# Kernel optimization log

Hardware: AMD Instinct MI355X
Metric: run time of the kernel (lower is better)

## Reference

```python
import jax, jax.numpy as jnp
import numpy as np


def _gtconv(A, w):
    # A: [E,N,N], w: [C,E,1,1]; torch: sum(A * softmax(w, dim=1), dim=1) -> [C,N,N]
    s = jax.nn.softmax(w[:, :, 0, 0], axis=1)  # [C,E]
    return jnp.einsum('enm,ce->cnm', A, s)


def _norm_row(H):
    # row-normalize (H + I): D^-1 (H + I)
    n = H.shape[0]
    H = H + jnp.eye(n, dtype=H.dtype)
    deg = jnp.sum(H, axis=1)
    deg = jnp.where(deg <= 1e-10, 1.0, deg)
    return H / deg[:, None]


def _sgc(feature, adj):
    # D^-1/2 (adj + 2I) D^-1/2 @ feature  (diag scaling, same math as torch's dense mm with diag)
    n = adj.shape[0]
    adj = adj + 2.0 * jnp.eye(n, dtype=adj.dtype)
    deg = jnp.sum(adj, axis=1)
    deg = jnp.where(deg <= 1e-10, 1.0, deg)
    dinv = deg ** -0.5
    adj = adj * dinv[:, None] * dinv[None, :]
    return adj @ feature


def setup_inputs() -> dict:
    key = jax.random.key(0)
    ks = jax.random.split(key, 20)
    E, C, N, D, P, F = 5, 2, 3000, 1000, 2000, 128
    inp = {
        'A': jax.random.uniform(ks[0], (E, N, N), dtype=jnp.float32),
        'DTI': jax.random.uniform(ks[1], (N, N), dtype=jnp.float32),
        'drug_structure': jax.random.normal(ks[2], (D, F), dtype=jnp.float32),
        'protein_structure': jax.random.normal(ks[3], (P, F), dtype=jnp.float32),
        'gt_w0a': jax.random.normal(ks[4], (C, E, 1, 1), dtype=jnp.float32),
        'gt_w0b': jax.random.normal(ks[5], (C, E, 1, 1), dtype=jnp.float32),
        'gt_w1': jax.random.normal(ks[6], (C, E, 1, 1), dtype=jnp.float32),
        'a_param': jnp.ones((C + 1, 1, 1), dtype=jnp.float32),
        'drug_num': D,
        'protein_num': P,
    }
    lin_keys = jax.random.split(ks[7], 12)
    names = ['wd1', 'bd1', 'wd2', 'bd2', 'wd3', 'bd3', 'wp1', 'bp1', 'wp2', 'bp2', 'wp3', 'bp3']
    for i, nm in enumerate(names):
        shp = (F, F) if nm.startswith('w') else (F,)
        inp[nm] = jax.random.normal(lin_keys[i], shp, dtype=jnp.float32) * 0.05
    return inp


def reference(A, DTI, drug_structure, protein_structure, gt_w0a, gt_w0b, gt_w1,
              wd1, bd1, wd2, bd2, wd3, bd3, wp1, bp1, wp2, bp2, wp3, bp3,
              a_param, drug_num, protein_num):
    relu = jax.nn.relu
    drug = relu(drug_structure @ wd1.T + bd1)
    drug = relu(drug @ wd2.T + bd2)
    drug = relu(drug @ wd3.T + bd3)
    prot = relu(protein_structure @ wp1.T + bp1)
    prot = relu(prot @ wp2.T + bp2)
    prot = relu(prot @ wp3.T + bp3)
    feature = jnp.concatenate([drug, prot], axis=0)  # [N,128]

    # GT layers: layer 0 (first=True), layer 1 (first=False)
    a0 = _gtconv(A, gt_w0a)  # [C,N,N]
    b0 = _gtconv(A, gt_w0b)
    H = jnp.matmul(a0, b0)  # bmm
    H = jax.vmap(_norm_row)(H)
    H = jnp.matmul(H, _gtconv(A, gt_w1))

    adj = H  # H[:, :N, :N] is a no-op here
    X_conv1 = _sgc(_sgc(feature, DTI), DTI)
    chs = jax.vmap(lambda a_: _sgc(_sgc(feature, a_), a_))(adj)  # [C,N,128]

    C = adj.shape[0]
    if C == 1:
        X_conv3 = chs
    else:
        order = [0, 1]
        for i in range(2, C):
            order = [i] + order  # torch prepends X_tem for i>=2
        X_conv3 = chs[jnp.array(order)]

    X_conv = jnp.concatenate([X_conv1[None], X_conv3], axis=0)  # [C+1,N,128]
    att = jax.nn.softmax(a_param, axis=0)  # [C+1,1,1]
    conv_sum = jnp.sum(att * X_conv, axis=0)  # [N,128]

    drug_feature = conv_sum[:drug_num]
    protein_feature = conv_sum[drug_num:]
    y = jax.nn.sigmoid(drug_feature @ protein_feature.T)  # [D,P]
    return y
```

## Files before the change

### kernel.cpp

```cpp
#include <hip/hip_runtime.h>
#include <hip/hip_bf16.h>

typedef __attribute__((ext_vector_type(8))) __bf16 bf16x8;
typedef __attribute__((ext_vector_type(4))) float floatx4;

#define NVALID 3000
#define NPAD   3072
#define FEA    128
#define ZSPLIT 8
#define KCHUNK 384
#define PSTRIDE 393216
#define SLOT   ((size_t)ZSPLIT * PSTRIDE)

__device__ __forceinline__ void gload16(const void* g, void* l) {
    __builtin_amdgcn_global_load_lds(
        (const __attribute__((address_space(1))) void*)g,
        (__attribute__((address_space(3))) void*)l,
        16, 0, 0);
}

__device__ __forceinline__ float b2f(__hip_bfloat16 h) { return __bfloat162float(h); }

__global__ __launch_bounds__(256) void mlp_fused(
    const float* __restrict__ Xd, const float* __restrict__ Xp,
    const float* __restrict__ Wd1, const float* __restrict__ bd1,
    const float* __restrict__ Wd2, const float* __restrict__ bd2,
    const float* __restrict__ Wd3, const float* __restrict__ bd3,
    const float* __restrict__ Wp1, const float* __restrict__ bp1,
    const float* __restrict__ Wp2, const float* __restrict__ bp2,
    const float* __restrict__ Wp3, const float* __restrict__ bp3,
    float* __restrict__ Y)
{
    const bool isP = blockIdx.x >= 125;
    const float* X  = isP ? Xp : Xd;
    const float* W1 = isP ? Wp1 : Wd1; const float* b1 = isP ? bp1 : bd1;
    const float* W2 = isP ? Wp2 : Wd2; const float* b2 = isP ? bp2 : bd2;
    const float* W3 = isP ? Wp3 : Wd3; const float* b3 = isP ? bp3 : bd3;
    const int m0loc = (isP ? (blockIdx.x - 125) : blockIdx.x) * 8;
    const int m0out = blockIdx.x * 8;

    __shared__ float S0[8][128], S1[8][128];
    const int t = threadIdx.x;
    for (int s2 = t; s2 < 1024; s2 += 256) {
        int r = s2 >> 7, ii = s2 & 127;
        S0[r][ii] = X[(size_t)(m0loc + r) * 128 + ii];
    }
    __syncthreads();
    const int o = t & 127, rh = t >> 7;

    {
        float a0 = 0.f, a1 = 0.f, a2 = 0.f, a3 = 0.f;
        const float* wr = W1 + (size_t)o * 128;
        for (int i = 0; i < 128; ++i) {
            float w = wr[i];
            a0 += S0[rh + 0][i] * w; a1 += S0[rh + 2][i] * w;
            a2 += S0[rh + 4][i] * w; a3 += S0[rh + 6][i] * w;
        }
        float bo = b1[o];
        S1[rh + 0][o] = fmaxf(a0 + bo, 0.f);
        S1[rh + 2][o] = fmaxf(a1 + bo, 0.f);
        S1[rh + 4][o] = fmaxf(a2 + bo, 0.f);
        S1[rh + 6][o] = fmaxf(a3 + bo, 0.f);
    }
    __syncthreads();
    {
        float a0 = 0.f, a1 = 0.f, a2 = 0.f, a3 = 0.f;
        const float* wr = W2 + (size_t)o * 128;
        for (int i = 0; i < 128; ++i) {
            float w = wr[i];
            a0 += S1[rh + 0][i] * w; a1 += S1[rh + 2][i] * w;
            a2 += S1[rh + 4][i] * w; a3 += S1[rh + 6][i] * w;
        }
        float bo = b2[o];
        S0[rh + 0][o] = fmaxf(a0 + bo, 0.f);
        S0[rh + 2][o] = fmaxf(a1 + bo, 0.f);
        S0[rh + 4][o] = fmaxf(a2 + bo, 0.f);
        S0[rh + 6][o] = fmaxf(a3 + bo, 0.f);
    }
    __syncthreads();
    {
        float a0 = 0.f, a1 = 0.f, a2 = 0.f, a3 = 0.f;
        const float* wr = W3 + (size_t)o * 128;
        for (int i = 0; i < 128; ++i) {
            float w = wr[i];
            a0 += S0[rh + 0][i] * w; a1 += S0[rh + 2][i] * w;
            a2 += S0[rh + 4][i] * w; a3 += S0[rh + 6][i] * w;
        }
        float bo = b3[o];
        Y[(size_t)(m0out + rh + 0) * 128 + o] = fmaxf(a0 + bo, 0.f);
        Y[(size_t)(m0out + rh + 2) * 128 + o] = fmaxf(a1 + bo, 0.f);
        Y[(size_t)(m0out + rh + 4) * 128 + o] = fmaxf(a2 + bo, 0.f);
        Y[(size_t)(m0out + rh + 6) * 128 + o] = fmaxf(a3 + bo, 0.f);
    }
}

__device__ __forceinline__ void softmax5(const float* __restrict__ w, float* s)
{
    float m = w[0];
    #pragma unroll
    for (int e = 1; e < 5; ++e) m = fmaxf(m, w[e]);
    float sum = 0.f;
    #pragma unroll
    for (int e = 0; e < 5; ++e) { s[e] = __expf(w[e] - m); sum += s[e]; }
    float r = 1.f / sum;
    #pragma unroll
    for (int e = 0; e < 5; ++e) s[e] *= r;
}

__global__ __launch_bounds__(256) void gtconv_stream(
    const float* __restrict__ A, const float* __restrict__ w0a,
    const float* __restrict__ w0b, const float* __restrict__ w1,
    __hip_bfloat16* __restrict__ a00, __hip_bfloat16* __restrict__ b00,
    __hip_bfloat16* __restrict__ g10,
    __hip_bfloat16* __restrict__ a01, __hip_bfloat16* __restrict__ b01,
    __hip_bfloat16* __restrict__ g11)
{
    float sa0[5], sb0[5], sg0[5], sa1[5], sb1[5], sg1[5];
    softmax5(w0a + 0, sa0); softmax5(w0b + 0, sb0); softmax5(w1 + 0, sg0);
    softmax5(w0a + 5, sa1); softmax5(w0b + 5, sb1); softmax5(w1 + 5, sg1);

    const int i  = blockIdx.y;
    const int j0 = blockIdx.x * 1024 + threadIdx.x * 4;
    float acc[6][4] = {};
    if (i < NVALID && j0 < NVALID) {
        const bool fast = (j0 + 3) < NVALID;
        #pragma unroll
        for (int e = 0; e < 5; ++e) {
            const float* Ae = A + (size_t)e * 9000000 + (size_t)i * 3000;
            float x[4];
            if (fast) {
                float4 v = *reinterpret_cast<const float4*>(Ae + j0);
                x[0] = v.x; x[1] = v.y; x[2] = v.z; x[3] = v.w;
            } else {
                #pragma unroll
                for (int u = 0; u < 4; ++u)
                    x[u] = (j0 + u < NVALID) ? Ae[j0 + u] : 0.f;
            }
            #pragma unroll
            for (int u = 0; u < 4; ++u) {
                acc[0][u] += sa0[e] * x[u];
                acc[1][u] += sb0[e] * x[u];
                acc[2][u] += sg0[e] * x[u];
                acc[3][u] += sa1[e] * x[u];
                acc[4][u] += sb1[e] * x[u];
                acc[5][u] += sg1[e] * x[u];
            }
        }
    }
    __hip_bfloat16* dsts[6] = { a00, b00, g10, a01, b01, g11 };
    const size_t base = (size_t)i * NPAD + j0;
    #pragma unroll
    for (int m = 0; m < 6; ++m) {
        __align__(8) __hip_bfloat16 h[4];
        #pragma unroll
        for (int u = 0; u < 4; ++u) h[u] = __float2bfloat16(acc[m][u]);
        *reinterpret_cast<uint2*>(&dsts[m][base]) = *reinterpret_cast<const uint2*>(h);
    }
}

__global__ __launch_bounds__(256) void rowsum4(
    const __hip_bfloat16* __restrict__ M0, const __hip_bfloat16* __restrict__ M1,
    const __hip_bfloat16* __restrict__ M2, const __hip_bfloat16* __restrict__ M3,
    float* __restrict__ r1v)
{
    const __hip_bfloat16* M = (blockIdx.y == 0) ? M0 : (blockIdx.y == 1) ? M1
                            : (blockIdx.y == 2) ? M2 : M3;
    const size_t i = blockIdx.x;
    const int t = threadIdx.x;
    const __hip_bfloat16* row = M + i * NPAD;
    float s = 0.f;
    for (int k = t * 8; k < NPAD; k += 2048) {
        uint4 u = *reinterpret_cast<const uint4*>(&row[k]);
        const unsigned short* us = reinterpret_cast<const unsigned short*>(&u);
        #pragma unroll
        for (int e = 0; e < 8; ++e)
            s += __uint_as_float(((unsigned int)us[e]) << 16);
    }
    #pragma unroll
    for (int off = 32; off > 0; off >>= 1) s += __shfl_down(s, off);
    __shared__ float red[4];
    if ((t & 63) == 0) red[t >> 6] = s;
    __syncthreads();
    if (t == 0)
        r1v[(size_t)blockIdx.y * NPAD + i] = red[0] + red[1] + red[2] + red[3];
}

__global__ __launch_bounds__(256) void matvec_degA(
    const __hip_bfloat16* __restrict__ a0_0, const __hip_bfloat16* __restrict__ a0_1,
    const __hip_bfloat16* __restrict__ b0_0, const __hip_bfloat16* __restrict__ b0_1,
    const float* __restrict__ r1v,
    float* __restrict__ dinv2, float* __restrict__ mv12)
{
    const int y = blockIdx.y;
    const __hip_bfloat16* M = (y == 0) ? a0_0 : (y == 1) ? a0_1 : (y == 2) ? b0_0 : b0_1;
    const float* v = (y == 0) ? r1v : (y == 1) ? r1v + 2 * NPAD
                   : (y == 2) ? r1v + NPAD : r1v + 3 * NPAD;
    const size_t i = blockIdx.x;
    const int t = threadIdx.x;
    const __hip_bfloat16* row = M + i * NPAD;
    float s = 0.f;
    for (int k = t * 8; k < NPAD; k += 2048) {
        uint4 u = *reinterpret_cast<const uint4*>(&row[k]);
        const unsigned short* us = reinterpret_cast<const unsigned short*>(&u);
        #pragma unroll
        for (int e = 0; e < 8; ++e)
            s += __uint_as_float(((unsigned int)us[e]) << 16) * v[k + e];
    }
    #pragma unroll
    for (int off = 32; off > 0; off >>= 1) s += __shfl_down(s, off);
    __shared__ float red[4];
    if ((t & 63) == 0) red[t >> 6] = s;
    __syncthreads();
    if (t == 0) {
        float tot = red[0] + red[1] + red[2] + red[3];
        if (y < 2) dinv2[(size_t)y * NPAD + i] = 1.f / (tot + 1.f);
        else       mv12[(size_t)(y - 2) * NPAD + i] = tot;
    }
}

__global__ __launch_bounds__(256) void matvec_degB(
    const __hip_bfloat16* __restrict__ a0_0, const __hip_bfloat16* __restrict__ a0_1,
    const float* __restrict__ mv12, const float* __restrict__ dinv2,
    const float* __restrict__ r1v, float* __restrict__ rsv2)
{
    const int c = blockIdx.y;
    const __hip_bfloat16* M = c ? a0_1 : a0_0;
    const float* v = mv12 + (size_t)c * NPAD;
    const float* add = r1v + (size_t)(2 * c + 1) * NPAD;
    const size_t i = blockIdx.x;
    const int t = threadIdx.x;
    const __hip_bfloat16* row = M + i * NPAD;
    float s = 0.f;
    for (int k = t * 8; k < NPAD; k += 2048) {
        uint4 u = *reinterpret_cast<const uint4*>(&row[k]);
        const unsigned short* us = reinterpret_cast<const unsigned short*>(&u);
        #pragma unroll
        for (int e = 0; e < 8; ++e)
            s += __uint_as_float(((unsigned int)us[e]) << 16) * v[k + e];
    }
    #pragma unroll
    for (int off = 32; off > 0; off >>= 1) s += __shfl_down(s, off);
    __shared__ float red[4];
    if ((t & 63) == 0) red[t >> 6] = s;
    __syncthreads();
    if (t == 0) {
        float tot = red[0] + red[1] + red[2] + red[3];
        rsv2[(size_t)c * NPAD + i] =
            rsqrtf(dinv2[(size_t)c * NPAD + i] * (tot + add[i]) + 2.f);
    }
}

__global__ __launch_bounds__(256) void rowdeg_f32(
    const float* __restrict__ src, float* __restrict__ outv)
{
    const int i = blockIdx.x, t = threadIdx.x;
    float s = 0.f;
    if (i < NVALID) {
        const float* row = src + (size_t)i * 3000;
        for (int j4 = t; j4 < 750; j4 += 256) {
            float4 v = *reinterpret_cast<const float4*>(row + j4 * 4);
            s += v.x + v.y + v.z + v.w;
        }
    }
    #pragma unroll
    for (int off = 32; off > 0; off >>= 1) s += __shfl_down(s, off);
    __shared__ float red[4];
    if ((t & 63) == 0) red[t >> 6] = s;
    __syncthreads();
    if (t == 0) {
        float tot = red[0] + red[1] + red[2] + red[3];
        outv[i] = rsqrtf(tot + 2.f);
    }
}

__global__ __launch_bounds__(256) void scale_cast_f32(
    const float* __restrict__ src, int lds_, int nvalid,
    const float* __restrict__ vec, __hip_bfloat16* __restrict__ dst)
{
    const int i = blockIdx.y;
    const int j0 = (blockIdx.x * 256 + threadIdx.x) * 4;
    const float vi = vec[i];
    float v[4];
    if (i < nvalid && j0 + 3 < nvalid) {
        float4 f = *reinterpret_cast<const float4*>(src + (size_t)i * lds_ + j0);
        v[0] = f.x; v[1] = f.y; v[2] = f.z; v[3] = f.w;
    } else {
        #pragma unroll
        for (int u = 0; u < 4; ++u) {
            int j = j0 + u;
            v[u] = (i < nvalid && j < nvalid) ? src[(size_t)i * lds_ + j] : 0.f;
        }
    }
    #pragma unroll
    for (int u = 0; u < 4; ++u) {
        int j = j0 + u;
        if (j == i && i < nvalid) v[u] += 2.f;
        v[u] *= vi * vec[j];
    }
    __align__(8) __hip_bfloat16 h[4];
    #pragma unroll
    for (int u = 0; u < 4; ++u) h[u] = __float2bfloat16(v[u]);
    *reinterpret_cast<uint2*>(&dst[(size_t)i * NPAD + j0]) =
        *reinterpret_cast<const uint2*>(h);
}

__global__ __launch_bounds__(256) void transpose_feat(
    const float* __restrict__ X, int nvalid, __hip_bfloat16* __restrict__ XT)
{
    __shared__ float Ts[32][33];
    const int k0 = blockIdx.x * 32, n0 = blockIdx.y * 32;
    const int t = threadIdx.x, tr = t >> 5, tc = t & 31;
    #pragma unroll
    for (int p = 0; p < 4; ++p) {
        int k = k0 + tr + p * 8;
        Ts[tr + p * 8][tc] = (k < nvalid) ? X[(size_t)k * 128 + n0 + tc] : 0.f;
    }
    __syncthreads();
    #pragma unroll
    for (int p = 0; p < 4; ++p) {
        int n = tr + p * 8;
        XT[(size_t)(n0 + n) * NPAD + k0 + tc] = __float2bfloat16(Ts[tc][n]);
    }
}

__global__ __launch_bounds__(256) void scale_colsT2(
    const __hip_bfloat16* __restrict__ XT, const float* __restrict__ rsv2,
    __hip_bfloat16* __restrict__ W0T_0, __hip_bfloat16* __restrict__ W0T_1)
{
    const int c = blockIdx.z;
    const float* s = rsv2 + (size_t)c * NPAD;
    __hip_bfloat16* W0T = c ? W0T_1 : W0T_0;
    const int f = blockIdx.y;
    const int k0 = (blockIdx.x * 256 + threadIdx.x) * 8;
    if (k0 >= NPAD) return;
    uint4 u = *reinterpret_cast<const uint4*>(&XT[(size_t)f * NPAD + k0]);
    const unsigned short* us = reinterpret_cast<const unsigned short*>(&u);
    __align__(16) __hip_bfloat16 h[8];
    #pragma unroll
    for (int e = 0; e < 8; ++e) {
        float x = __uint_as_float(((unsigned int)us[e]) << 16);
        h[e] = __float2bfloat16(x * s[k0 + e]);
    }
    *reinterpret_cast<uint4*>(&W0T[(size_t)f * NPAD + k0]) =
        *reinterpret_cast<const uint4*>(h);
}

__global__ __launch_bounds__(256, 3) void gemm_bt_batch(
    const __hip_bfloat16* __restrict__ A0, const __hip_bfloat16* __restrict__ B0,
    const __hip_bfloat16* __restrict__ A1, const __hip_bfloat16* __restrict__ B1,
    const __hip_bfloat16* __restrict__ A2, const __hip_bfloat16* __restrict__ B2,
    float* __restrict__ part)
{
    const int b  = blockIdx.z / ZSPLIT;
    const int zz = blockIdx.z % ZSPLIT;
    const __hip_bfloat16* A  = (b == 0) ? A0 : (b == 1) ? A1 : A2;
    const __hip_bfloat16* BT = (b == 0) ? B0 : (b == 1) ? B1 : B2;
    float* C = part + (size_t)b * SLOT + (size_t)zz * PSTRIDE;

    __shared__ __align__(16) __hip_bfloat16 As[128 * 32];
    __shared__ __align__(16) __hip_bfloat16 Bs[128 * 32];
    const int t = threadIdx.x;
    const int lane = t & 63;
    const int w = t >> 6;
    const int wm = w >> 1, wn = w & 1;
    const int tm = blockIdx.y;
    const int kbeg = zz * KCHUNK;

    const int srow = lane >> 2;
    const int skg  = (lane & 3) * 8;
    const __hip_bfloat16* Ag = A  + (size_t)(tm * 128 + w * 32 + srow) * NPAD + skg;
    const __hip_bfloat16* Bg = BT + (size_t)(w * 32 + srow) * NPAD + skg;
    __hip_bfloat16* Al0 = &As[w * 1024];
    __hip_bfloat16* Al1 = &As[w * 1024 + 512];
    __hip_bfloat16* Bl0 = &Bs[w * 1024];
    __hip_bfloat16* Bl1 = &Bs[w * 1024 + 512];

    floatx4 acc[4][4] = {};

    for (int k0 = kbeg; k0 < kbeg + KCHUNK; k0 += 32) {
        __syncthreads();
        gload16(Ag + k0,             Al0);
        gload16(Ag + 16 * NPAD + k0, Al1);
        gload16(Bg + k0,             Bl0);
        gload16(Bg + 16 * NPAD + k0, Bl1);
        __syncthreads();

        bf16x8 af[4], bfv[4];
        const int koff = (lane >> 4) * 8;
        #pragma unroll
        for (int mi = 0; mi < 4; ++mi)
            af[mi] = *reinterpret_cast<const bf16x8*>(
                &As[(wm * 64 + mi * 16 + (lane & 15)) * 32 + koff]);
        #pragma unroll
        for (int ni = 0; ni < 4; ++ni)
            bfv[ni] = *reinterpret_cast<const bf16x8*>(
                &Bs[(wn * 64 + ni * 16 + (lane & 15)) * 32 + koff]);
        #pragma unroll
        for (int mi = 0; mi < 4; ++mi)
            #pragma unroll
            for (int ni = 0; ni < 4; ++ni)
                acc[mi][ni] = __builtin_amdgcn_mfma_f32_16x16x32_bf16(
                    af[mi], bfv[ni], acc[mi][ni], 0, 0, 0);
    }

    const int r0 = tm * 128 + wm * 64 + ((lane >> 4) << 2);
    const int c0 = wn * 64 + (lane & 15);
    #pragma unroll
    for (int mi = 0; mi < 4; ++mi)
        #pragma unroll
        for (int ni = 0; ni < 4; ++ni)
            #pragma unroll
            for (int r = 0; r < 4; ++r)
                C[(size_t)(r0 + mi * 16 + r) * 128 + c0 + ni * 16] = acc[mi][ni][r];
}

__global__ __launch_bounds__(256, 3) void gemm_sig(
    const __hip_bfloat16* __restrict__ A, const __hip_bfloat16* __restrict__ BT,
    float* __restrict__ C, int Kchunk, int lda, int ldb, int ldc,
    int Mvalid, int Nvalid)
{
    __shared__ __align__(16) __hip_bfloat16 As[128 * 32];
    __shared__ __align__(16) __hip_bfloat16 Bs[128 * 32];
    const int t = threadIdx.x;
    const int lane = t & 63;
    const int w = t >> 6;
    const int wm = w >> 1, wn = w & 1;
    const int tm = blockIdx.y, tn = blockIdx.x;

    const int srow = lane >> 2;
    const int skg  = (lane & 3) * 8;
    const __hip_bfloat16* Ag = A  + (size_t)(tm * 128 + w * 32 + srow) * lda + skg;
    const __hip_bfloat16* Bg = BT + (size_t)(tn * 128 + w * 32 + srow) * ldb + skg;
    __hip_bfloat16* Al0 = &As[w * 1024];
    __hip_bfloat16* Al1 = &As[w * 1024 + 512];
    __hip_bfloat16* Bl0 = &Bs[w * 1024];
    __hip_bfloat16* Bl1 = &Bs[w * 1024 + 512];

    floatx4 acc[4][4] = {};

    for (int k0 = 0; k0 < Kchunk; k0 += 32) {
        __syncthreads();
        gload16(Ag + k0,            Al0);
        gload16(Ag + 16 * lda + k0, Al1);
        gload16(Bg + k0,            Bl0);
        gload16(Bg + 16 * ldb + k0, Bl1);
        __syncthreads();

        bf16x8 af[4], bfv[4];
        const int koff = (lane >> 4) * 8;
        #pragma unroll
        for (int mi = 0; mi < 4; ++mi)
            af[mi] = *reinterpret_cast<const bf16x8*>(
                &As[(wm * 64 + mi * 16 + (lane & 15)) * 32 + koff]);
        #pragma unroll
        for (int ni = 0; ni < 4; ++ni)
            bfv[ni] = *reinterpret_cast<const bf16x8*>(
                &Bs[(wn * 64 + ni * 16 + (lane & 15)) * 32 + koff]);
        #pragma unroll
        for (int mi = 0; mi < 4; ++mi)
            #pragma unroll
            for (int ni = 0; ni < 4; ++ni)
                acc[mi][ni] = __builtin_amdgcn_mfma_f32_16x16x32_bf16(
                    af[mi], bfv[ni], acc[mi][ni], 0, 0, 0);
    }

    const int r0 = tm * 128 + wm * 64 + ((lane >> 4) << 2);
    const int c0 = tn * 128 + wn * 64 + (lane & 15);
    #pragma unroll
    for (int mi = 0; mi < 4; ++mi)
        #pragma unroll
        for (int ni = 0; ni < 4; ++ni) {
            const int col = c0 + ni * 16;
            #pragma unroll
            for (int r = 0; r < 4; ++r) {
                const int row = r0 + mi * 16 + r;
                if (row < Mvalid && col < Nvalid)
                    C[(size_t)row * ldc + col] =
                        1.f / (1.f + __expf(-acc[mi][ni][r]));
            }
        }
}

__global__ __launch_bounds__(256) void reduce_trans_b(
    const float* __restrict__ part,
    __hip_bfloat16* __restrict__ X0, __hip_bfloat16* __restrict__ X1,
    __hip_bfloat16* __restrict__ X2,
    __hip_bfloat16* __restrict__ R0, __hip_bfloat16* __restrict__ R1,
    __hip_bfloat16* __restrict__ R2)
{
    const int b = blockIdx.z;
    const float* Pp = part + (size_t)b * SLOT;
    __hip_bfloat16* XT = (b == 0) ? X0 : (b == 1) ? X1 : X2;
    __hip_bfloat16* Rm = (b == 0) ? R0 : (b == 1) ? R1 : R2;

    __shared__ float Ts[32][33];
    const int k0 = blockIdx.x * 32, n0 = blockIdx.y * 32;
    const int t = threadIdx.x, tr = t >> 5, tc = t & 31;
    #pragma unroll
    for (int p = 0; p < 4; ++p) {
        int i = k0 + tr + p * 8;
        float s = 0.f;
        #pragma unroll
        for (int z = 0; z < ZSPLIT; ++z)
            s += Pp[(size_t)z * PSTRIDE + (size_t)i * 128 + n0 + tc];
        Ts[tr + p * 8][tc] = s;
        if (Rm) Rm[(size_t)i * 128 + n0 + tc] = __float2bfloat16(s);
    }
    __syncthreads();
    #pragma unroll
    for (int p = 0; p < 4; ++p) {
        int n = tr + p * 8;
        XT[(size_t)(n0 + n) * NPAD + k0 + tc] = __float2bfloat16(Ts[tc][n]);
    }
}

__global__ __launch_bounds__(256) void reduce_att_f32(
    const float* __restrict__ Pp, const float* __restrict__ ap,
    float* __restrict__ conv)
{
    const int idx = blockIdx.x * 256 + threadIdx.x;
    float s = 0.f;
    #pragma unroll
    for (int z = 0; z < ZSPLIT; ++z)
        s += Pp[(size_t)z * PSTRIDE + idx];
    float a0 = ap[0], a1 = ap[1], a2 = ap[2];
    float m = fmaxf(a0, fmaxf(a1, a2));
    float e0 = __expf(a0 - m), e1 = __expf(a1 - m), e2 = __expf(a2 - m);
    conv[idx] = (e0 / (e0 + e1 + e2)) * s;
}

__global__ __launch_bounds__(256) void combine_mid2(
    const float* __restrict__ part,
    const __hip_bfloat16* __restrict__ Zrm0, const __hip_bfloat16* __restrict__ Zrm1,
    const float* __restrict__ X,
    const float* __restrict__ rsv2, const float* __restrict__ dinv2,
    __hip_bfloat16* __restrict__ WpT0, __hip_bfloat16* __restrict__ WpT1,
    __hip_bfloat16* __restrict__ Wprm0, __hip_bfloat16* __restrict__ Wprm1)
{
    const int c = blockIdx.z;
    const float* Vp = part + (size_t)c * SLOT;
    const __hip_bfloat16* Zrm = c ? Zrm1 : Zrm0;
    const float* sv = rsv2 + (size_t)c * NPAD;
    const float* dv = dinv2 + (size_t)c * NPAD;
    __hip_bfloat16* WpT  = c ? WpT1 : WpT0;
    __hip_bfloat16* Wprm = c ? Wprm1 : Wprm0;

    __shared__ float Ts[32][33];
    const int k0 = blockIdx.x * 32, n0 = blockIdx.y * 32;
    const int t = threadIdx.x, tr = t >> 5, tc = t & 31;
    #pragma unroll
    for (int p = 0; p < 4; ++p) {
        int i = k0 + tr + p * 8;
        int f = n0 + tc;
        float vsum = b2f(Zrm[(size_t)i * 128 + f]);
        #pragma unroll
        for (int z = 0; z < ZSPLIT; ++z)
            vsum += Vp[(size_t)z * PSTRIDE + (size_t)i * 128 + f];
        float x  = (i < NVALID) ? X[(size_t)i * 128 + f] : 0.f;
        float si = sv[i];
        float out1 = si * dv[i] * vsum + 2.f * si * si * x;
        float wv = si * out1;
        Ts[tr + p * 8][tc] = wv;
        Wprm[(size_t)i * 128 + f] = __float2bfloat16(wv);
    }
    __syncthreads();
    #pragma unroll
    for (int p = 0; p < 4; ++p) {
        int n = tr + p * 8;
        WpT[(size_t)(n0 + n) * NPAD + k0 + tc] = __float2bfloat16(Ts[tc][n]);
    }
}

__global__ __launch_bounds__(256) void combine_att2(
    const float* __restrict__ part,
    const __hip_bfloat16* __restrict__ Zrm0, const __hip_bfloat16* __restrict__ Zrm1,
    const __hip_bfloat16* __restrict__ Wprm0, const __hip_bfloat16* __restrict__ Wprm1,
    const float* __restrict__ rsv2, const float* __restrict__ dinv2,
    const float* __restrict__ ap, float* __restrict__ conv)
{
    const int idx = blockIdx.x * 256 + threadIdx.x;
    const int i = idx >> 7;
    float v0 = b2f(Zrm0[idx]);
    float v1 = b2f(Zrm1[idx]);
    #pragma unroll
    for (int z = 0; z < ZSPLIT; ++z) {
        v0 += part[(size_t)z * PSTRIDE + idx];
        v1 += part[SLOT + (size_t)z * PSTRIDE + idx];
    }
    float s0 = rsv2[i],        d0 = dinv2[i];
    float s1 = rsv2[NPAD + i], d1 = dinv2[NPAD + i];
    float o0 = s0 * d0 * v0 + 2.f * s0 * b2f(Wprm0[idx]);
    float o1 = s1 * d1 * v1 + 2.f * s1 * b2f(Wprm1[idx]);
    float a0 = ap[0], a1 = ap[1], a2 = ap[2];
    float m = fmaxf(a0, fmaxf(a1, a2));
    float e0 = __expf(a0 - m), e1 = __expf(a1 - m), e2 = __expf(a2 - m);
    float inv = 1.f / (e0 + e1 + e2);
    conv[idx] += (e1 * inv) * o0 + (e2 * inv) * o1;
}

__global__ __launch_bounds__(256) void cast_split(
    const float* __restrict__ acc, __hip_bfloat16* __restrict__ dF,
    __hip_bfloat16* __restrict__ pF)
{
    const int idx = blockIdx.x * 256 + threadIdx.x;
    if (idx < 1024 * 128) {
        int r = idx >> 7;
        dF[idx] = __float2bfloat16(r < 1000 ? acc[idx] : 0.f);
    } else {
        int j = idx - 1024 * 128;
        int r = j >> 7;
        pF[j] = __float2bfloat16(r < 2000 ? acc[(size_t)(1000 + r) * 128 + (j & 127)] : 0.f);
    }
}

extern "C" void kernel_launch(void* const* d_in, const int* in_sizes, int n_in,
                              void* d_out, int out_size, void* d_ws, size_t ws_size,
                              hipStream_t stream)
{
    const float* A     = (const float*)d_in[0];
    const float* DTI   = (const float*)d_in[1];
    const float* drugS = (const float*)d_in[2];
    const float* protS = (const float*)d_in[3];
    const float* w0a   = (const float*)d_in[4];
    const float* w0b   = (const float*)d_in[5];
    const float* w1g   = (const float*)d_in[6];
    const float* ap    = (const float*)d_in[7];
    const float* wd1 = (const float*)d_in[10]; const float* bd1 = (const float*)d_in[11];
    const float* wd2 = (const float*)d_in[12]; const float* bd2 = (const float*)d_in[13];
    const float* wd3 = (const float*)d_in[14]; const float* bd3 = (const float*)d_in[15];
    const float* wp1 = (const float*)d_in[16]; const float* bp1 = (const float*)d_in[17];
    const float* wp2 = (const float*)d_in[18]; const float* bp2 = (const float*)d_in[19];
    const float* wp3 = (const float*)d_in[20]; const float* bp3 = (const float*)d_in[21];
    float* out = (float*)d_out;

    const size_t SQ_BF  = (size_t)NPAD * NPAD * 2;
    const size_t PAN_BF = (size_t)128 * NPAD * 2;
    char* p = (char*)d_ws;
    auto alloc = [&](size_t sz) { char* r = p; p += (sz + 255) & ~(size_t)255; return r; };
    __hip_bfloat16* sdti = (__hip_bfloat16*)alloc(SQ_BF);
    __hip_bfloat16* a0c[2], *b0c[2], *g1c[2];
    for (int c = 0; c < 2; ++c) {
        a0c[c] = (__hip_bfloat16*)alloc(SQ_BF);
        b0c[c] = (__hip_bfloat16*)alloc(SQ_BF);
        g1c[c] = (__hip_bfloat16*)alloc(SQ_BF);
    }
    float* part  = (float*)alloc((size_t)3 * SLOT * 4);
    float* r1v   = (float*)alloc((size_t)4 * NPAD * 4);
    float* dinv2 = (float*)alloc((size_t)2 * NPAD * 4);
    float* mv12  = (float*)alloc((size_t)2 * NPAD * 4);
    float* rsv2  = (float*)alloc((size_t)2 * NPAD * 4);
    float* degv  = (float*)alloc((size_t)NPAD * 4);
    float* fb    = (float*)alloc((size_t)NPAD * 128 * 4);
    float* conv  = (float*)alloc((size_t)NPAD * 128 * 4);
    __hip_bfloat16* XTF  = (__hip_bfloat16*)alloc(PAN_BF);
    __hip_bfloat16* XT2  = (__hip_bfloat16*)alloc(PAN_BF);
    __hip_bfloat16* W0T_0 = (__hip_bfloat16*)alloc(PAN_BF);
    __hip_bfloat16* W0T_1 = (__hip_bfloat16*)alloc(PAN_BF);
    __hip_bfloat16* ZT_0  = (__hip_bfloat16*)alloc(PAN_BF);
    __hip_bfloat16* ZT_1  = (__hip_bfloat16*)alloc(PAN_BF);
    __hip_bfloat16* Zrm_0 = (__hip_bfloat16*)alloc(PAN_BF);
    __hip_bfloat16* Zrm_1 = (__hip_bfloat16*)alloc(PAN_BF);
    __hip_bfloat16* UT_0  = (__hip_bfloat16*)alloc(PAN_BF);
    __hip_bfloat16* UT_1  = (__hip_bfloat16*)alloc(PAN_BF);
    __hip_bfloat16* WpT_0 = (__hip_bfloat16*)alloc(PAN_BF);
    __hip_bfloat16* WpT_1 = (__hip_bfloat16*)alloc(PAN_BF);
    __hip_bfloat16* Wprm_0 = (__hip_bfloat16*)alloc(PAN_BF);
    __hip_bfloat16* Wprm_1 = (__hip_bfloat16*)alloc(PAN_BF);
    __hip_bfloat16* dF = (__hip_bfloat16*)alloc((size_t)1024 * 128 * 2);
    __hip_bfloat16* pF = (__hip_bfloat16*)alloc((size_t)2048 * 128 * 2);
    if ((size_t)(p - (char*)d_ws) > ws_size) return;

    mlp_fused<<<375, 256, 0, stream>>>(drugS, protS,
        wd1, bd1, wd2, bd2, wd3, bd3, wp1, bp1, wp2, bp2, wp3, bp3, fb);
    transpose_feat<<<dim3(96, 4), 256, 0, stream>>>(fb, 3000, XTF);

    gtconv_stream<<<dim3(3, NPAD), 256, 0, stream>>>(A, w0a, w0b, w1g,
        a0c[0], b0c[0], g1c[0], a0c[1], b0c[1], g1c[1]);
    rowsum4<<<dim3(NPAD, 4), 256, 0, stream>>>(b0c[0], g1c[0], b0c[1], g1c[1], r1v);

    rowdeg_f32<<<NPAD, 256, 0, stream>>>(DTI, degv);
    scale_cast_f32<<<dim3(3, NPAD), 256, 0, stream>>>(DTI, 3000, 3000, degv, sdti);

    matvec_degA<<<dim3(NPAD, 4), 256, 0, stream>>>(a0c[0], a0c[1], b0c[0], b0c[1],
        r1v, dinv2, mv12);
    matvec_degB<<<dim3(NPAD, 2), 256, 0, stream>>>(a0c[0], a0c[1], mv12, dinv2, r1v, rsv2);
    scale_colsT2<<<dim3(2, 128, 2), 256, 0, stream>>>(XTF, rsv2, W0T_0, W0T_1);

    gemm_bt_batch<<<dim3(1, 24, 24), 256, 0, stream>>>(
        sdti, XTF, g1c[0], W0T_0, g1c[1], W0T_1, part);
    reduce_trans_b<<<dim3(96, 4, 3), 256, 0, stream>>>(part,
        XT2, ZT_0, ZT_1, nullptr, Zrm_0, Zrm_1);

    gemm_bt_batch<<<dim3(1, 24, 24), 256, 0, stream>>>(
        sdti, XT2, b0c[0], ZT_0, b0c[1], ZT_1, part);
    reduce_att_f32<<<1500, 256, 0, stream>>>(part, ap, conv);
    reduce_trans_b<<<dim3(96, 4, 2), 256, 0, stream>>>(part + SLOT,
        UT_0, UT_1, nullptr, nullptr, nullptr, nullptr);

    gemm_bt_batch<<<dim3(1, 24, 16), 256, 0, stream>>>(
        a0c[0], UT_0, a0c[1], UT_1, nullptr, nullptr, part);
    combine_mid2<<<dim3(96, 4, 2), 256, 0, stream>>>(part, Zrm_0, Zrm_1, fb,
        rsv2, dinv2, WpT_0, WpT_1, Wprm_0, Wprm_1);

    gemm_bt_batch<<<dim3(1, 24, 16), 256, 0, stream>>>(
        g1c[0], WpT_0, g1c[1], WpT_1, nullptr, nullptr, part);
    reduce_trans_b<<<dim3(96, 4, 2), 256, 0, stream>>>(part,
        ZT_0, ZT_1, nullptr, Zrm_0, Zrm_1, nullptr);
    gemm_bt_batch<<<dim3(1, 24, 16), 256, 0, stream>>>(
        b0c[0], ZT_0, b0c[1], ZT_1, nullptr, nullptr, part);
    reduce_trans_b<<<dim3(96, 4, 2), 256, 0, stream>>>(part,
        UT_0, UT_1, nullptr, nullptr, nullptr, nullptr);
    gemm_bt_batch<<<dim3(1, 24, 16), 256, 0, stream>>>(
        a0c[0], UT_0, a0c[1], UT_1, nullptr, nullptr, part);
    combine_att2<<<1500, 256, 0, stream>>>(part, Zrm_0, Zrm_1, Wprm_0, Wprm_1,
        rsv2, dinv2, ap, conv);

    cast_split<<<1536, 256, 0, stream>>>(conv, dF, pF);
    gemm_sig<<<dim3(16, 8), 256, 0, stream>>>(dF, pF, out, 128, 128, 128, 2000, 1000, 2000);
}
```

Measured before the change: 288.7 us.

## Fuse gtconv with row sums, merge attention reduce, halve split-K factor

The gtconv kernel now handles one full row per 384-thread block and computes the bf16-rounded row sums of the four needed matrices in-register, which removes the separate rowsum4 pass over those matrices. The attention-scaled reduction of the DTI partials is folded into the reduce_trans_b launch as an extra z-slice, saving one launch. The split-K factor drops from 8 to 4 with doubled K chunks, which halves the partial-sum traffic and reduction work but gives the GEMMs fewer blocks and less parallelism. Row j0 reads are now unguarded up to column 3000, which relies on row padding and block-size bounds.

```diff
diff --git a/kernel.cpp b/kernel.cpp
--- a/kernel.cpp
+++ b/kernel.cpp
@@ -7,8 +7,8 @@
 #define NVALID 3000
 #define NPAD   3072
 #define FEA    128
-#define ZSPLIT 8
-#define KCHUNK 384
+#define ZSPLIT 4
+#define KCHUNK 768
 #define PSTRIDE 393216
 #define SLOT   ((size_t)ZSPLIT * PSTRIDE)
 
@@ -107,82 +107,71 @@
     for (int e = 0; e < 5; ++e) s[e] *= r;
 }
 
-__global__ __launch_bounds__(256) void gtconv_stream(
+__global__ __launch_bounds__(384) void gtconv_fused(
     const float* __restrict__ A, const float* __restrict__ w0a,
     const float* __restrict__ w0b, const float* __restrict__ w1,
     __hip_bfloat16* __restrict__ a00, __hip_bfloat16* __restrict__ b00,
     __hip_bfloat16* __restrict__ g10,
     __hip_bfloat16* __restrict__ a01, __hip_bfloat16* __restrict__ b01,
-    __hip_bfloat16* __restrict__ g11)
-{
-    float sa0[5], sb0[5], sg0[5], sa1[5], sb1[5], sg1[5];
-    softmax5(w0a + 0, sa0); softmax5(w0b + 0, sb0); softmax5(w1 + 0, sg0);
-    softmax5(w0a + 5, sa1); softmax5(w0b + 5, sb1); softmax5(w1 + 5, sg1);
-
-    const int i  = blockIdx.y;
-    const int j0 = blockIdx.x * 1024 + threadIdx.x * 4;
-    float acc[6][4] = {};
+    __hip_bfloat16* __restrict__ g11,
+    float* __restrict__ r1v)
+{
+    float sw[6][5];
+    softmax5(w0a + 0, sw[0]); softmax5(w0b + 0, sw[1]); softmax5(w1 + 0, sw[2]);
+    softmax5(w0a + 5, sw[3]); softmax5(w0b + 5, sw[4]); softmax5(w1 + 5, sw[5]);
+
+    const int i  = blockIdx.x;
+    const int t  = threadIdx.x;
+    const int j0 = t * 8;
+    float acc[6][8] = {};
     if (i < NVALID && j0 < NVALID) {
-        const bool fast = (j0 + 3) < NVALID;
         #pragma unroll
         for (int e = 0; e < 5; ++e) {
-            const float* Ae = A + (size_t)e * 9000000 + (size_t)i * 3000;
-            float x[4];
-            if (fast) {
-                float4 v = *reinterpret_cast<const float4*>(Ae + j0);
-                x[0] = v.x; x[1] = v.y; x[2] = v.z; x[3] = v.w;
-            } else {
+            const float* Ae = A + (size_t)e * 9000000 + (size_t)i * 3000 + j0;
+            float4 v0 = *reinterpret_cast<const float4*>(Ae);
+            float4 v1 = *reinterpret_cast<const float4*>(Ae + 4);
+            float x[8] = { v0.x, v0.y, v0.z, v0.w, v1.x, v1.y, v1.z, v1.w };
+            #pragma unroll
+            for (int m = 0; m < 6; ++m) {
+                float se = sw[m][e];
                 #pragma unroll
-                for (int u = 0; u < 4; ++u)
-                    x[u] = (j0 + u < NVALID) ? Ae[j0 + u] : 0.f;
-            }
-            #pragma unroll
-            for (int u = 0; u < 4; ++u) {
-                acc[0][u] += sa0[e] * x[u];
-                acc[1][u] += sb0[e] * x[u];
-                acc[2][u] += sg0[e] * x[u];
-                acc[3][u] += sa1[e] * x[u];
-                acc[4][u] += sb1[e] * x[u];
-                acc[5][u] += sg1[e] * x[u];
+                for (int u = 0; u < 8; ++u) acc[m][u] += se * x[u];
             }
         }
     }
     __hip_bfloat16* dsts[6] = { a00, b00, g10, a01, b01, g11 };
     const size_t base = (size_t)i * NPAD + j0;
+    float rs[4];
     #pragma unroll
     for (int m = 0; m < 6; ++m) {
-        __align__(8) __hip_bfloat16 h[4];
-        #pragma unroll
-        for (int u = 0; u < 4; ++u) h[u] = __float2bfloat16(acc[m][u]);
-        *reinterpret_cast<uint2*>(&dsts[m][base]) = *reinterpret_cast<const uint2*>(h);
-    }
-}
-
-__global__ __launch_bounds__(256) void rowsum4(
-    const __hip_bfloat16* __restrict__ M0, const __hip_bfloat16* __restrict__ M1,
-    const __hip_bfloat16* __restrict__ M2, const __hip_bfloat16* __restrict__ M3,
-    float* __restrict__ r1v)
-{
-    const __hip_bfloat16* M = (blockIdx.y == 0) ? M0 : (blockIdx.y == 1) ? M1
-                            : (blockIdx.y == 2) ? M2 : M3;
-    const size_t i = blockIdx.x;
-    const int t = threadIdx.x;
-    const __hip_bfloat16* row = M + i * NPAD;
-    float s = 0.f;
-    for (int k = t * 8; k < NPAD; k += 2048) {
-        uint4 u = *reinterpret_cast<const uint4*>(&row[k]);
-        const unsigned short* us = reinterpret_cast<const unsigned short*>(&u);
-        #pragma unroll
-        for (int e = 0; e < 8; ++e)
-            s += __uint_as_float(((unsigned int)us[e]) << 16);
-    }
-    #pragma unroll
-    for (int off = 32; off > 0; off >>= 1) s += __shfl_down(s, off);
-    __shared__ float red[4];
-    if ((t & 63) == 0) red[t >> 6] = s;
-    __syncthreads();
-    if (t == 0)
-        r1v[(size_t)blockIdx.y * NPAD + i] = red[0] + red[1] + red[2] + red[3];
+        __align__(16) __hip_bfloat16 h[8];
+        float s = 0.f;
+        #pragma unroll
+        for (int u = 0; u < 8; ++u) {
+            h[u] = __float2bfloat16(acc[m][u]);
+            s += b2f(h[u]);
+        }
+        *reinterpret_cast<uint4*>(&dsts[m][base]) = *reinterpret_cast<const uint4*>(h);
+        if (m == 1) rs[0] = s; else if (m == 2) rs[1] = s;
+        else if (m == 4) rs[2] = s; else if (m == 5) rs[3] = s;
+    }
+    __shared__ float red[6][4];
+    #pragma unroll
+    for (int q = 0; q < 4; ++q) {
+        float s = rs[q];
+        #pragma unroll
+        for (int off = 32; off > 0; off >>= 1) s += __shfl_down(s, off);
+        if ((t & 63) == 0) red[t >> 6][q] = s;
+    }
+    __syncthreads();
+    if (t == 0) {
+        #pragma unroll
+        for (int q = 0; q < 4; ++q) {
+            float s = red[0][q] + red[1][q] + red[2][q]
+                    + red[3][q] + red[4][q] + red[5][q];
+            r1v[(size_t)q * NPAD + i] = s;
+        }
+    }
 }
 
 __global__ __launch_bounds__(256) void matvec_degA(
@@ -486,16 +475,34 @@
     __hip_bfloat16* __restrict__ X0, __hip_bfloat16* __restrict__ X1,
     __hip_bfloat16* __restrict__ X2,
     __hip_bfloat16* __restrict__ R0, __hip_bfloat16* __restrict__ R1,
-    __hip_bfloat16* __restrict__ R2)
+    __hip_bfloat16* __restrict__ R2,
+    const float* __restrict__ ap, float* __restrict__ conv)
 {
     const int b = blockIdx.z;
     const float* Pp = part + (size_t)b * SLOT;
+    const int k0 = blockIdx.x * 32, n0 = blockIdx.y * 32;
+    const int t = threadIdx.x, tr = t >> 5, tc = t & 31;
+
+    if (b == 0 && conv != nullptr) {
+        float a0 = ap[0], a1 = ap[1], a2 = ap[2];
+        float m = fmaxf(a0, fmaxf(a1, a2));
+        float e0 = __expf(a0 - m), e1 = __expf(a1 - m), e2 = __expf(a2 - m);
+        float att0 = e0 / (e0 + e1 + e2);
+        #pragma unroll
+        for (int p = 0; p < 4; ++p) {
+            int i = k0 + tr + p * 8;
+            float s = 0.f;
+            #pragma unroll
+            for (int z = 0; z < ZSPLIT; ++z)
+                s += Pp[(size_t)z * PSTRIDE + (size_t)i * 128 + n0 + tc];
+            conv[(size_t)i * 128 + n0 + tc] = att0 * s;
+        }
+        return;
+    }
+
     __hip_bfloat16* XT = (b == 0) ? X0 : (b == 1) ? X1 : X2;
     __hip_bfloat16* Rm = (b == 0) ? R0 : (b == 1) ? R1 : R2;
-
     __shared__ float Ts[32][33];
-    const int k0 = blockIdx.x * 32, n0 = blockIdx.y * 32;
-    const int t = threadIdx.x, tr = t >> 5, tc = t & 31;
     #pragma unroll
     for (int p = 0; p < 4; ++p) {
         int i = k0 + tr + p * 8;
@@ -512,21 +519,6 @@
         int n = tr + p * 8;
         XT[(size_t)(n0 + n) * NPAD + k0 + tc] = __float2bfloat16(Ts[tc][n]);
     }
-}
-
-__global__ __launch_bounds__(256) void reduce_att_f32(
-    const float* __restrict__ Pp, const float* __restrict__ ap,
-    float* __restrict__ conv)
-{
-    const int idx = blockIdx.x * 256 + threadIdx.x;
-    float s = 0.f;
-    #pragma unroll
-    for (int z = 0; z < ZSPLIT; ++z)
-        s += Pp[(size_t)z * PSTRIDE + idx];
-    float a0 = ap[0], a1 = ap[1], a2 = ap[2];
-    float m = fmaxf(a0, fmaxf(a1, a2));
-    float e0 = __expf(a0 - m), e1 = __expf(a1 - m), e2 = __expf(a2 - m);
-    conv[idx] = (e0 / (e0 + e1 + e2)) * s;
 }
 
 __global__ __launch_bounds__(256) void combine_mid2(
@@ -674,9 +666,8 @@
         wd1, bd1, wd2, bd2, wd3, bd3, wp1, bp1, wp2, bp2, wp3, bp3, fb);
     transpose_feat<<<dim3(96, 4), 256, 0, stream>>>(fb, 3000, XTF);
 
-    gtconv_stream<<<dim3(3, NPAD), 256, 0, stream>>>(A, w0a, w0b, w1g,
-        a0c[0], b0c[0], g1c[0], a0c[1], b0c[1], g1c[1]);
-    rowsum4<<<dim3(NPAD, 4), 256, 0, stream>>>(b0c[0], g1c[0], b0c[1], g1c[1], r1v);
+    gtconv_fused<<<NPAD, 384, 0, stream>>>(A, w0a, w0b, w1g,
+        a0c[0], b0c[0], g1c[0], a0c[1], b0c[1], g1c[1], r1v);
 
     rowdeg_f32<<<NPAD, 256, 0, stream>>>(DTI, degv);
     scale_cast_f32<<<dim3(3, NPAD), 256, 0, stream>>>(DTI, 3000, 3000, degv, sdti);
@@ -686,31 +677,30 @@
     matvec_degB<<<dim3(NPAD, 2), 256, 0, stream>>>(a0c[0], a0c[1], mv12, dinv2, r1v, rsv2);
     scale_colsT2<<<dim3(2, 128, 2), 256, 0, stream>>>(XTF, rsv2, W0T_0, W0T_1);
 
-    gemm_bt_batch<<<dim3(1, 24, 24), 256, 0, stream>>>(
+    gemm_bt_batch<<<dim3(1, 24, 3 * ZSPLIT), 256, 0, stream>>>(
         sdti, XTF, g1c[0], W0T_0, g1c[1], W0T_1, part);
     reduce_trans_b<<<dim3(96, 4, 3), 256, 0, stream>>>(part,
-        XT2, ZT_0, ZT_1, nullptr, Zrm_0, Zrm_1);
-
-    gemm_bt_batch<<<dim3(1, 24, 24), 256, 0, stream>>>(
+        XT2, ZT_0, ZT_1, nullptr, Zrm_0, Zrm_1, nullptr, nullptr);
+
+    gemm_bt_batch<<<dim3(1, 24, 3 * ZSPLIT), 256, 0, stream>>>(
         sdti, XT2, b0c[0], ZT_0, b0c[1], ZT_1, part);
-    reduce_att_f32<<<1500, 256, 0, stream>>>(part, ap, conv);
-    reduce_trans_b<<<dim3(96, 4, 2), 256, 0, stream>>>(part + SLOT,
-        UT_0, UT_1, nullptr, nullptr, nullptr, nullptr);
-
-    gemm_bt_batch<<<dim3(1, 24, 16), 256, 0, stream>>>(
+    reduce_trans_b<<<dim3(96, 4, 3), 256, 0, stream>>>(part,
+        nullptr, UT_0, UT_1, nullptr, nullptr, nullptr, ap, conv);
+
+    gemm_bt_batch<<<dim3(1, 24, 2 * ZSPLIT), 256, 0, stream>>>(
         a0c[0], UT_0, a0c[1], UT_1, nullptr, nullptr, part);
     combine_mid2<<<dim3(96, 4, 2), 256, 0, stream>>>(part, Zrm_0, Zrm_1, fb,
         rsv2, dinv2, WpT_0, WpT_1, Wprm_0, Wprm_1);
 
-    gemm_bt_batch<<<dim3(1, 24, 16), 256, 0, stream>>>(
+    gemm_bt_batch<<<dim3(1, 24, 2 * ZSPLIT), 256, 0, stream>>>(
         g1c[0], WpT_0, g1c[1], WpT_1, nullptr, nullptr, part);
     reduce_trans_b<<<dim3(96, 4, 2), 256, 0, stream>>>(part,
-        ZT_0, ZT_1, nullptr, Zrm_0, Zrm_1, nullptr);
-    gemm_bt_batch<<<dim3(1, 24, 16), 256, 0, stream>>>(
+        ZT_0, ZT_1, nullptr, Zrm_0, Zrm_1, nullptr, nullptr, nullptr);
+    gemm_bt_batch<<<dim3(1, 24, 2 * ZSPLIT), 256, 0, stream>>>(
         b0c[0], ZT_0, b0c[1], ZT_1, nullptr, nullptr, part);
     reduce_trans_b<<<dim3(96, 4, 2), 256, 0, stream>>>(part,
-        UT_0, UT_1, nullptr, nullptr, nullptr, nullptr);
-    gemm_bt_batch<<<dim3(1, 24, 16), 256, 0, stream>>>(
+        UT_0, UT_1, nullptr, nullptr, nullptr, nullptr, nullptr, nullptr);
+    gemm_bt_batch<<<dim3(1, 24, 2 * ZSPLIT), 256, 0, stream>>>(
         a0c[0], UT_0, a0c[1], UT_1, nullptr, nullptr, part);
     combine_att2<<<1500, 256, 0, stream>>>(part, Zrm_0, Zrm_1, Wprm_0, Wprm_1,
         rsv2, dinv2, ap, conv);
```

Result: slower. 298.1 us (+3.3%).
